# Optimization experiments

Hardware: AMD Instinct MI355X
Metric: run time of the kernel (lower is better)

Reference implementation:

```python
import jax, jax.numpy as jnp
import numpy as np

N_NODES = 50000
N_EDGES = 800000
D_IN = 128
D_HID = 128
D_OUT = 40
NUM_LAYERS = 2


def _sage_conv(x, src, dst, W_l, b_l, W_r, num_nodes):
    # PyG SAGEConv (aggr='mean'): out = lin_l(mean_{j in N(i)} x_j) + lin_r(x_i)
    msg = x[src]                                              # [E, d] gather
    agg = jax.ops.segment_sum(msg, dst, num_segments=num_nodes)  # [N, d] scatter-add
    deg = jax.ops.segment_sum(jnp.ones_like(dst, dtype=x.dtype), dst,
                              num_segments=num_nodes)
    agg = agg / jnp.clip(deg, 1.0)[:, None]                   # mean (deg>=1 clamp)
    return agg @ W_l.T + b_l + x @ W_r.T


def setup_inputs() -> dict:
    key = jax.random.key(0)
    ks = jax.random.split(key, 10)
    x = jax.random.normal(ks[0], (N_NODES, D_IN), dtype=jnp.float32)
    edge_index = jax.random.randint(ks[1], (2, N_EDGES), 0, N_NODES, dtype=jnp.int64)
    s = 1.0 / np.sqrt(D_IN)
    W1_l = jax.random.uniform(ks[2], (D_HID, D_IN), jnp.float32, -s, s)
    b1_l = jax.random.uniform(ks[3], (D_HID,), jnp.float32, -s, s)
    W1_r = jax.random.uniform(ks[4], (D_HID, D_IN), jnp.float32, -s, s)
    sh = 1.0 / np.sqrt(D_HID)
    W2_l = jax.random.uniform(ks[5], (D_HID, D_HID), jnp.float32, -sh, sh)
    b2_l = jax.random.uniform(ks[6], (D_HID,), jnp.float32, -sh, sh)
    W2_r = jax.random.uniform(ks[7], (D_HID, D_HID), jnp.float32, -sh, sh)
    sc = 1.0 / np.sqrt(D_HID * NUM_LAYERS)
    W_lin = jax.random.uniform(ks[8], (D_OUT, D_HID * NUM_LAYERS), jnp.float32, -sc, sc)
    b_lin = jax.random.uniform(ks[9], (D_OUT,), jnp.float32, -sc, sc)
    return {"x": x, "edge_index": edge_index,
            "W1_l": W1_l, "b1_l": b1_l, "W1_r": W1_r,
            "W2_l": W2_l, "b2_l": b2_l, "W2_r": W2_r,
            "W_lin": W_lin, "b_lin": b_lin}


def reference(x, edge_index, W1_l, b1_l, W1_r, W2_l, b2_l, W2_r, W_lin, b_lin):
    src, dst = edge_index[0], edge_index[1]
    n = x.shape[0]
    h1 = jax.nn.relu(_sage_conv(x, src, dst, W1_l, b1_l, W1_r, n))   # dropout: eval mode -> identity
    h2 = jax.nn.relu(_sage_conv(h1, src, dst, W2_l, b2_l, W2_r, n))
    h_cat = jnp.concatenate([h1, h2], axis=1)                        # [N, 2*hid]
    logits = h_cat @ W_lin.T + b_lin                                 # [N, out]
    return jax.nn.log_softmax(logits, axis=1)
```

## Files before the change

### kernel.cpp

```cpp
#include <hip/hip_runtime.h>
#include <math.h>

#define N_NODES 50000
#define N_EDGES 800000
#define D 128
#define NBLK 196
#define GATHER_BLOCKS 2048

typedef __attribute__((ext_vector_type(8))) short bf16x8;
typedef __attribute__((ext_vector_type(4))) float f32x4;
typedef __attribute__((ext_vector_type(4))) unsigned int u32x4;

static __device__ __forceinline__ unsigned short f2bf(float f) {
    unsigned int u = __float_as_uint(f);
    u = (u + 0x7fffu + ((u >> 16) & 1u)) >> 16;
    return (unsigned short)u;
}
static __device__ __forceinline__ float bf2f(unsigned short h) {
    return __uint_as_float(((unsigned int)h) << 16);
}

__global__ void prep_deg_kernel(const int* __restrict__ dst, int* __restrict__ deg,
                                int* __restrict__ rank,
                                const float* __restrict__ x,
                                const float* __restrict__ W1l, const float* __restrict__ W1r,
                                const float* __restrict__ W2l, const float* __restrict__ W2r,
                                const float* __restrict__ Wlin,
                                unsigned short* __restrict__ xhi, unsigned short* __restrict__ xlo,
                                unsigned short* __restrict__ W1hi, unsigned short* __restrict__ W1lo,
                                unsigned short* __restrict__ W2hi, unsigned short* __restrict__ W2lo,
                                unsigned short* __restrict__ WLhi, unsigned short* __restrict__ WLlo) {
    int b = blockIdx.x, tid = threadIdx.x;
    if (b < 3125) {
        int e = b * 256 + tid;
        rank[e] = atomicAdd(&deg[dst[e]], 1);
    } else if (b < 9375) {
        int i = ((b - 3125) * 256 + tid) * 4;
        float4 v = *(const float4*)(x + i);
        ushort4 h, l;
        h.x = f2bf(v.x); l.x = f2bf(v.x - bf2f(h.x));
        h.y = f2bf(v.y); l.y = f2bf(v.y - bf2f(h.y));
        h.z = f2bf(v.z); l.z = f2bf(v.z - bf2f(h.z));
        h.w = f2bf(v.w); l.w = f2bf(v.w - bf2f(h.w));
        *(ushort4*)(xhi + i) = h;
        *(ushort4*)(xlo + i) = l;
    } else if (b < 9503) {
        int isW2 = (b >= 9439);
        const float* A = isW2 ? W2l : W1l;
        const float* B = isW2 ? W2r : W1r;
        unsigned short* hi = isW2 ? W2hi : W1hi;
        unsigned short* lo = isW2 ? W2lo : W1lo;
        int f = (b - (isW2 ? 9439 : 9375)) * 2 + (tid >> 7);
        int t = tid & 127;
        float va = A[f * 128 + t], vb = B[f * 128 + t];
        unsigned short ha = f2bf(va), hb = f2bf(vb);
        hi[f * 256 + t]       = ha;
        hi[f * 256 + 128 + t] = hb;
        lo[f * 256 + t]       = f2bf(va - bf2f(ha));
        lo[f * 256 + 128 + t] = f2bf(vb - bf2f(hb));
    } else {
        int f = b - 9503;
        float v = (f < 40) ? Wlin[f * 256 + tid] : 0.f;
        unsigned short h = f2bf(v);
        WLhi[f * 256 + tid] = h;
        WLlo[f * 256 + tid] = f2bf(v - bf2f(h));
    }
}

__global__ void scan_partial(const int* __restrict__ deg, int* __restrict__ bsum) {
    __shared__ int wt[4];
    int tid = threadIdx.x, lane = tid & 63, wv = tid >> 6;
    int idx = blockIdx.x * 256 + tid;
    int v = (idx < N_NODES) ? deg[idx] : 0;
    int s = v;
    #pragma unroll
    for (int o = 1; o < 64; o <<= 1) s += __shfl_xor(s, o, 64);
    if (lane == 0) wt[wv] = s;
    __syncthreads();
    if (tid == 0) bsum[blockIdx.x] = wt[0] + wt[1] + wt[2] + wt[3];
}

__global__ void scan_write(const int* __restrict__ deg, const int* __restrict__ bsum,
                           int* __restrict__ rowptr) {
    __shared__ int wt[4], wt2[4];
    int tid = threadIdx.x, lane = tid & 63, wv = tid >> 6;
    int v0 = (tid < blockIdx.x) ? bsum[tid] : 0;
    int s0 = v0;
    #pragma unroll
    for (int o = 1; o < 64; o <<= 1) s0 += __shfl_xor(s0, o, 64);
    if (lane == 0) wt2[wv] = s0;
    int idx = blockIdx.x * 256 + tid;
    int v = (idx < N_NODES) ? deg[idx] : 0;
    int s = v;
    #pragma unroll
    for (int o = 1; o < 64; o <<= 1) { int t = __shfl_up(s, o, 64); if (lane >= o) s += t; }
    if (lane == 63) wt[wv] = s;
    __syncthreads();
    int boff = wt2[0] + wt2[1] + wt2[2] + wt2[3];
    #pragma unroll
    for (int w = 0; w < 4; w++) boff += (w < wv) ? wt[w] : 0;
    int excl = boff + s - v;
    if (idx < N_NODES) rowptr[idx] = excl;
    if (idx == 0) rowptr[N_NODES] = N_EDGES;
}

__global__ void bucket_kernel(const int* __restrict__ src, const int* __restrict__ dst,
                              const int* __restrict__ rowptr, const int* __restrict__ rank,
                              int* __restrict__ srcs_sorted) {
    int e = blockIdx.x * blockDim.x + threadIdx.x;
    if (e < N_EDGES) {
        srcs_sorted[rowptr[dst[e]] + rank[e]] = src[e];
    }
}

__global__ __launch_bounds__(256, 8) void gather_mean(
    const int* __restrict__ srcs, const int* __restrict__ rowptr,
    const unsigned short* __restrict__ Shi,
    unsigned short* __restrict__ Aghi, unsigned short* __restrict__ Aglo)
{
    const int tid = threadIdx.x;
    const int wv = tid >> 6, lane = tid & 63;
    const int g = lane >> 4, q = lane & 15;
    const int qb = q << 4;
    const char* xb = (const char*)Shi;
    const int wid = blockIdx.x * 4 + wv;
    const int NW = GATHER_BLOCKS * 4;
    #pragma unroll 1
    for (int p = wid; p < N_NODES / 2; p += NW) {
        const int nA = 2 * p, nB = 2 * p + 1;
        const int begA = rowptr[nA];
        const int endA = rowptr[nA + 1];
        const int endB = rowptr[nB + 1];
        const int begB = endA;
        const int degA = endA - begA, degB = endB - begB;
        float ax[4] = {0,0,0,0}, ay[4] = {0,0,0,0};
        float bx[4] = {0,0,0,0}, by[4] = {0,0,0,0};
        int nsA = (degA + 63) >> 6, nsB = (degB + 63) >> 6;
        int nsmax = max(nsA, nsB);
        #pragma unroll 1
        for (int st = 0; st < nsmax; st++) {
            int svA = 0, svB = 0, nbA = 0, nbB = 0;
            if (st < nsA) {
                int sb = begA + (st << 6);
                nbA = min(64, endA - sb);
                svA = srcs[min(sb + lane, endA - 1)];
            }
            if (st < nsB) {
                int sb = begB + (st << 6);
                nbB = min(64, endB - sb);
                svB = srcs[min(sb + lane, endB - 1)];
            }
            int itA = (nbA + 3) >> 2, itB = (nbB + 3) >> 2;
            int itmax = max(itA, itB);
            #pragma unroll 2
            for (int b = 0; b < itmax; b++) {
                int ei = (b << 2) + g;
                if (b < itA) {
                    unsigned sv = (unsigned)__shfl(svA, ei, 64);
                    u32x4 v = *(const u32x4*)(xb + ((sv << 8) + qb));
                    v.x = (ei < nbA) ? v.x : 0u;
                    v.y = (ei < nbA) ? v.y : 0u;
                    v.z = (ei < nbA) ? v.z : 0u;
                    v.w = (ei < nbA) ? v.w : 0u;
                    ax[0] += __uint_as_float(v.x << 16); ay[0] += __uint_as_float(v.x & 0xffff0000u);
                    ax[1] += __uint_as_float(v.y << 16); ay[1] += __uint_as_float(v.y & 0xffff0000u);
                    ax[2] += __uint_as_float(v.z << 16); ay[2] += __uint_as_float(v.z & 0xffff0000u);
                    ax[3] += __uint_as_float(v.w << 16); ay[3] += __uint_as_float(v.w & 0xffff0000u);
                }
                if (b < itB) {
                    unsigned sv = (unsigned)__shfl(svB, ei, 64);
                    u32x4 v = *(const u32x4*)(xb + ((sv << 8) + qb));
                    v.x = (ei < nbB) ? v.x : 0u;
                    v.y = (ei < nbB) ? v.y : 0u;
                    v.z = (ei < nbB) ? v.z : 0u;
                    v.w = (ei < nbB) ? v.w : 0u;
                    bx[0] += __uint_as_float(v.x << 16); by[0] += __uint_as_float(v.x & 0xffff0000u);
                    bx[1] += __uint_as_float(v.y << 16); by[1] += __uint_as_float(v.y & 0xffff0000u);
                    bx[2] += __uint_as_float(v.z << 16); by[2] += __uint_as_float(v.z & 0xffff0000u);
                    bx[3] += __uint_as_float(v.w << 16); by[3] += __uint_as_float(v.w & 0xffff0000u);
                }
            }
        }
        #pragma unroll
        for (int d = 0; d < 4; d++) {
            ax[d] += __shfl_xor(ax[d], 16, 64); ax[d] += __shfl_xor(ax[d], 32, 64);
            ay[d] += __shfl_xor(ay[d], 16, 64); ay[d] += __shfl_xor(ay[d], 32, 64);
            bx[d] += __shfl_xor(bx[d], 16, 64); bx[d] += __shfl_xor(bx[d], 32, 64);
            by[d] += __shfl_xor(by[d], 16, 64); by[d] += __shfl_xor(by[d], 32, 64);
        }
        if (g == 0) {
            float invA = 1.0f / fmaxf((float)degA, 1.0f);
            float invB = 1.0f / fmaxf((float)degB, 1.0f);
            u32x4 ha, la, hb, lb;
            #pragma unroll
            for (int d = 0; d < 4; d++) {
                float sx = ax[d] * invA, sy = ay[d] * invA;
                unsigned short h0 = f2bf(sx), h1 = f2bf(sy);
                unsigned short l0 = f2bf(sx - bf2f(h0)), l1 = f2bf(sy - bf2f(h1));
                ha[d] = (unsigned)h0 | ((unsigned)h1 << 16);
                la[d] = (unsigned)l0 | ((unsigned)l1 << 16);
                float tx = bx[d] * invB, ty = by[d] * invB;
                unsigned short h2 = f2bf(tx), h3 = f2bf(ty);
                unsigned short l2 = f2bf(tx - bf2f(h2)), l3 = f2bf(ty - bf2f(h3));
                hb[d] = (unsigned)h2 | ((unsigned)h3 << 16);
                lb[d] = (unsigned)l2 | ((unsigned)l3 << 16);
            }
            *(u32x4*)(Aghi + (size_t)nA * D + q * 8) = ha;
            *(u32x4*)(Aglo + (size_t)nA * D + q * 8) = la;
            *(u32x4*)(Aghi + (size_t)nB * D + q * 8) = hb;
            *(u32x4*)(Aglo + (size_t)nB * D + q * 8) = lb;
        }
    }
}

template<bool FINAL>
__global__ __launch_bounds__(256, 4) void gemm_layer(
    const unsigned short* __restrict__ Aghi, const unsigned short* __restrict__ Aglo,
    const unsigned short* __restrict__ A2hi, const unsigned short* __restrict__ A2lo,
    const unsigned short* __restrict__ Whi, const unsigned short* __restrict__ Wlo,
    const float* __restrict__ bias,
    unsigned short* __restrict__ Ohi, unsigned short* __restrict__ Olo,
    const unsigned short* __restrict__ WLhi, const unsigned short* __restrict__ WLlo,
    const float* __restrict__ blin, float* __restrict__ out)
{
    __shared__ unsigned short Wl[2][8192];

    const int tid = threadIdx.x;
    const int wv = tid >> 6, lane = tid & 63;
    const int nb0 = blockIdx.x * 32;
    const int m = lane & 15, quad = lane >> 4;
    const int gg = wv & 1, tp = wv >> 1;
    const int nodec = min(nb0 + gg * 16 + m, N_NODES - 1);

    bf16x8 a1h[4], a1l[4], a2h[4], a2l[4];
    {
        const unsigned short* r1h = Aghi + (size_t)nodec * D + quad * 8;
        const unsigned short* r1l = Aglo + (size_t)nodec * D + quad * 8;
        const unsigned short* r2h = A2hi + (size_t)nodec * D + quad * 8;
        const unsigned short* r2l = A2lo + (size_t)nodec * D + quad * 8;
        #pragma unroll
        for (int ks = 0; ks < 4; ks++) {
            a1h[ks] = *(const bf16x8*)(r1h + ks * 32);
            a1l[ks] = *(const bf16x8*)(r1l + ks * 32);
            a2h[ks] = *(const bf16x8*)(r2h + ks * 32);
            a2l[ks] = *(const bf16x8*)(r2l + ks * 32);
        }
    }
    #pragma unroll
    for (int ks = 0; ks < 4; ks++) {
        asm volatile("" : "+v"(a1h[ks]), "+v"(a1l[ks]), "+v"(a2h[ks]), "+v"(a2l[ks]));
    }

    #pragma unroll 1
    for (int fq = 0; fq < 4; fq++) {
        const int f0 = fq * 32;
        if (fq) __syncthreads();
        #pragma unroll
        for (int itS = 0; itS < 8; itS++) {
            int c = tid + itS * 256;
            int plane = c >> 10;
            int w3 = c & 1023;
            int nt = w3 >> 9, w2 = w3 & 511;
            int ks = w2 >> 6, lidx = w2 & 63;
            int mm = lidx >> 2, qq = lidx & 3;
            const unsigned short* base = plane ? Wlo : Whi;
            const unsigned short* gp = base + (size_t)(f0 + nt * 16 + mm) * 256 + ks * 32 + qq * 8;
            *(bf16x8*)&Wl[plane][(size_t)w3 * 8] = *(const bf16x8*)gp;
        }
        __syncthreads();

        int f = f0 + tp * 16 + m;
        f32x4 acc0 = {0.f, 0.f, 0.f, 0.f};
        f32x4 acc1 = {0.f, 0.f, 0.f, 0.f};
        f32x4 acc2 = {0.f, 0.f, 0.f, 0.f};
        #pragma unroll
        for (int ks = 0; ks < 8; ks++) {
            int idx = (((tp * 8 + ks) << 6) + (m * 4 + quad)) * 8;
            bf16x8 bh = *(const bf16x8*)&Wl[0][idx];
            bf16x8 bl = *(const bf16x8*)&Wl[1][idx];
            bf16x8 ah = (ks < 4) ? a1h[ks] : a2h[ks - 4];
            bf16x8 al = (ks < 4) ? a1l[ks] : a2l[ks - 4];
            acc0 = __builtin_amdgcn_mfma_f32_16x16x32_bf16(ah, bh, acc0, 0, 0, 0);
            acc1 = __builtin_amdgcn_mfma_f32_16x16x32_bf16(ah, bl, acc1, 0, 0, 0);
            acc2 = __builtin_amdgcn_mfma_f32_16x16x32_bf16(al, bh, acc2, 0, 0, 0);
        }
        float bv = bias[f];
        #pragma unroll
        for (int r = 0; r < 4; r++) {
            int lrow = gg * 16 + quad * 4 + r;
            int nrow = nb0 + lrow;
            float v = fmaxf((acc0[r] + (acc1[r] + acc2[r])) + bv, 0.f);
            unsigned short h = f2bf(v);
            unsigned short l = f2bf(v - bf2f(h));
            if (nrow < N_NODES) {
                Ohi[(size_t)nrow * D + f] = h;
                Olo[(size_t)nrow * D + f] = l;
            }
        }
    }

    if (!FINAL) return;

    __syncthreads();
    float* stats = (float*)Wl;
    bf16x8 a3h[4], a3l[4];
    {
        const unsigned short* r3h = Ohi + (size_t)nodec * D + quad * 8;
        const unsigned short* r3l = Olo + (size_t)nodec * D + quad * 8;
        #pragma unroll
        for (int ks = 0; ks < 4; ks++) {
            a3h[ks] = *(const bf16x8*)(r3h + ks * 32);
            a3l[ks] = *(const bf16x8*)(r3l + ks * 32);
        }
    }
    const int ntiles = (tp == 0) ? 2 : 1;
    float res[2][4];
    #pragma unroll
    for (int t = 0; t < 2; t++) {
        if (t >= ntiles) break;
        int nt = (tp == 0) ? t : 2;
        int f = nt * 16 + m;
        const unsigned short* whirow = WLhi + (size_t)f * 256 + quad * 8;
        const unsigned short* wlorow = WLlo + (size_t)f * 256 + quad * 8;
        f32x4 acc0 = {0.f, 0.f, 0.f, 0.f};
        f32x4 acc1 = {0.f, 0.f, 0.f, 0.f};
        f32x4 acc2 = {0.f, 0.f, 0.f, 0.f};
        #pragma unroll
        for (int ks = 0; ks < 8; ks++) {
            bf16x8 bh = *(const bf16x8*)(whirow + ks * 32);
            bf16x8 bl = *(const bf16x8*)(wlorow + ks * 32);
            bf16x8 ah = (ks < 4) ? a2h[ks] : a3h[ks - 4];
            bf16x8 al = (ks < 4) ? a2l[ks] : a3l[ks - 4];
            acc0 = __builtin_amdgcn_mfma_f32_16x16x32_bf16(ah, bh, acc0, 0, 0, 0);
            acc1 = __builtin_amdgcn_mfma_f32_16x16x32_bf16(ah, bl, acc1, 0, 0, 0);
            acc2 = __builtin_amdgcn_mfma_f32_16x16x32_bf16(al, bh, acc2, 0, 0, 0);
        }
        float bv = (f < 40) ? blin[f] : 0.f;
        #pragma unroll
        for (int r = 0; r < 4; r++) res[t][r] = (acc0[r] + (acc1[r] + acc2[r])) + bv;
    }
    #pragma unroll
    for (int r = 0; r < 4; r++) {
        float pm = -INFINITY;
        #pragma unroll
        for (int t = 0; t < 2; t++) {
            if (t >= ntiles) break;
            int f = ((tp == 0) ? t : 2) * 16 + m;
            if (f < 40) pm = fmaxf(pm, res[t][r]);
        }
        #pragma unroll
        for (int o = 8; o > 0; o >>= 1) pm = fmaxf(pm, __shfl_xor(pm, o, 64));
        if (m == 0) stats[tp * 64 + gg * 16 + quad * 4 + r] = pm;
    }
    __syncthreads();
    float gm[4];
    #pragma unroll
    for (int r = 0; r < 4; r++) {
        int row = gg * 16 + quad * 4 + r;
        gm[r] = fmaxf(stats[row], stats[64 + row]);
        float ps = 0.f;
        #pragma unroll
        for (int t = 0; t < 2; t++) {
            if (t >= ntiles) break;
            int f = ((tp == 0) ? t : 2) * 16 + m;
            if (f < 40) ps += expf(res[t][r] - gm[r]);
        }
        #pragma unroll
        for (int o = 8; o > 0; o >>= 1) ps += __shfl_xor(ps, o, 64);
        if (m == 0) stats[128 + tp * 64 + row] = ps;
    }
    __syncthreads();
    #pragma unroll
    for (int r = 0; r < 4; r++) {
        int row = gg * 16 + quad * 4 + r;
        int nrow = nb0 + row;
        if (nrow >= N_NODES) continue;
        float lse = gm[r] + logf(stats[128 + row] + stats[192 + row]);
        #pragma unroll
        for (int t = 0; t < 2; t++) {
            if (t >= ntiles) break;
            int f = ((tp == 0) ? t : 2) * 16 + m;
            if (f < 40) out[(size_t)nrow * 40 + f] = res[t][r] - lse;
        }
    }
}

extern "C" void kernel_launch(void* const* d_in, const int* in_sizes, int n_in,
                              void* d_out, int out_size, void* d_ws, size_t ws_size,
                              hipStream_t stream) {
    const float* x     = (const float*)d_in[0];
    const int*   ei    = (const int*)d_in[1];
    const int*   src   = ei;
    const int*   dst   = ei + N_EDGES;
    const float* W1_l  = (const float*)d_in[2];
    const float* b1_l  = (const float*)d_in[3];
    const float* W1_r  = (const float*)d_in[4];
    const float* W2_l  = (const float*)d_in[5];
    const float* b2_l  = (const float*)d_in[6];
    const float* W2_r  = (const float*)d_in[7];
    const float* W_lin = (const float*)d_in[8];
    const float* b_lin = (const float*)d_in[9];
    float* out = (float*)d_out;

    const size_t nd = (size_t)N_NODES * D;
    unsigned short* xhi  = (unsigned short*)d_ws;
    unsigned short* xlo  = xhi + nd;
    unsigned short* h1hi = xlo + nd;
    unsigned short* h1lo = h1hi + nd;
    unsigned short* W1hi = h1lo + nd;
    unsigned short* W1lo = W1hi + 128 * 256;
    unsigned short* W2hi = W1lo + 128 * 256;
    unsigned short* W2lo = W2hi + 128 * 256;
    unsigned short* WLhi = W2lo + 128 * 256;
    unsigned short* WLlo = WLhi + 48 * 256;
    int* deg    = (int*)(WLlo + 48 * 256);
    int* rowptr = deg + N_NODES;
    int* rank   = rowptr + N_NODES + 1;
    int* srcs_sorted = rank + N_EDGES;
    int* bsum   = srcs_sorted + N_EDGES;
    unsigned short* aghi = (unsigned short*)(bsum + NBLK);
    unsigned short* aglo = aghi + nd;
    unsigned short* h2hi = aglo + nd;
    unsigned short* h2lo = h2hi + nd;

    hipMemsetAsync(deg, 0, N_NODES * sizeof(int), stream);
    prep_deg_kernel<<<9551, 256, 0, stream>>>(dst, deg, rank, x, W1_l, W1_r, W2_l, W2_r, W_lin,
                                              xhi, xlo, W1hi, W1lo, W2hi, W2lo, WLhi, WLlo);

    scan_partial<<<NBLK, 256, 0, stream>>>(deg, bsum);
    scan_write<<<NBLK, 256, 0, stream>>>(deg, bsum, rowptr);
    bucket_kernel<<<(N_EDGES + 255) / 256, 256, 0, stream>>>(src, dst, rowptr, rank, srcs_sorted);

    const int lblk = (N_NODES + 31) / 32;

    gather_mean<<<GATHER_BLOCKS, 256, 0, stream>>>(srcs_sorted, rowptr, xhi, aghi, aglo);
    gemm_layer<false><<<lblk, 256, 0, stream>>>(aghi, aglo, xhi, xlo,
                                                W1hi, W1lo, b1_l, h1hi, h1lo,
                                                nullptr, nullptr, nullptr, nullptr);
    gather_mean<<<GATHER_BLOCKS, 256, 0, stream>>>(srcs_sorted, rowptr, h1hi, aghi, aglo);
    gemm_layer<true><<<lblk, 256, 0, stream>>>(aghi, aglo, h1hi, h1lo,
                                               W2hi, W2lo, b2_l, h2hi, h2lo,
                                               WLhi, WLlo, b_lin, out);
}
```

Measured before the change: 302.7 us.

## Make GEMM persistent per feature-quarter and split classifier into separate kernel

```diff
diff --git a/kernel.cpp b/kernel.cpp
--- a/kernel.cpp
+++ b/kernel.cpp
@@ -6,6 +6,8 @@
 #define D 128
 #define NBLK 196
 #define GATHER_BLOCKS 2048
+#define NTILES 1563
+#define GEMM_CHUNKS 256
 
 typedef __attribute__((ext_vector_type(8))) short bf16x8;
 typedef __attribute__((ext_vector_type(4))) float f32x4;
@@ -213,63 +215,60 @@
     }
 }
 
-template<bool FINAL>
 __global__ __launch_bounds__(256, 4) void gemm_layer(
     const unsigned short* __restrict__ Aghi, const unsigned short* __restrict__ Aglo,
     const unsigned short* __restrict__ A2hi, const unsigned short* __restrict__ A2lo,
     const unsigned short* __restrict__ Whi, const unsigned short* __restrict__ Wlo,
     const float* __restrict__ bias,
-    unsigned short* __restrict__ Ohi, unsigned short* __restrict__ Olo,
-    const unsigned short* __restrict__ WLhi, const unsigned short* __restrict__ WLlo,
-    const float* __restrict__ blin, float* __restrict__ out)
+    unsigned short* __restrict__ Ohi, unsigned short* __restrict__ Olo)
 {
     __shared__ unsigned short Wl[2][8192];
 
     const int tid = threadIdx.x;
     const int wv = tid >> 6, lane = tid & 63;
-    const int nb0 = blockIdx.x * 32;
     const int m = lane & 15, quad = lane >> 4;
     const int gg = wv & 1, tp = wv >> 1;
-    const int nodec = min(nb0 + gg * 16 + m, N_NODES - 1);
-
-    bf16x8 a1h[4], a1l[4], a2h[4], a2l[4];
-    {
-        const unsigned short* r1h = Aghi + (size_t)nodec * D + quad * 8;
-        const unsigned short* r1l = Aglo + (size_t)nodec * D + quad * 8;
-        const unsigned short* r2h = A2hi + (size_t)nodec * D + quad * 8;
-        const unsigned short* r2l = A2lo + (size_t)nodec * D + quad * 8;
-        #pragma unroll
-        for (int ks = 0; ks < 4; ks++) {
-            a1h[ks] = *(const bf16x8*)(r1h + ks * 32);
-            a1l[ks] = *(const bf16x8*)(r1l + ks * 32);
-            a2h[ks] = *(const bf16x8*)(r2h + ks * 32);
-            a2l[ks] = *(const bf16x8*)(r2l + ks * 32);
-        }
-    }
-    #pragma unroll
-    for (int ks = 0; ks < 4; ks++) {
-        asm volatile("" : "+v"(a1h[ks]), "+v"(a1l[ks]), "+v"(a2h[ks]), "+v"(a2l[ks]));
-    }
+    const int fq = blockIdx.x & 3;
+    const int chunk = blockIdx.x >> 2;
+    const int f0 = fq * 32;
+
+    #pragma unroll
+    for (int itS = 0; itS < 8; itS++) {
+        int c = tid + itS * 256;
+        int plane = c >> 10;
+        int w3 = c & 1023;
+        int nt = w3 >> 9, w2 = w3 & 511;
+        int ks = w2 >> 6, lidx = w2 & 63;
+        int mm = lidx >> 2, qq = lidx & 3;
+        const unsigned short* base = plane ? Wlo : Whi;
+        const unsigned short* gp = base + (size_t)(f0 + nt * 16 + mm) * 256 + ks * 32 + qq * 8;
+        *(bf16x8*)&Wl[plane][(size_t)w3 * 8] = *(const bf16x8*)gp;
+    }
+    __syncthreads();
+
+    const int f = f0 + tp * 16 + m;
+    const float bv = bias[f];
 
     #pragma unroll 1
-    for (int fq = 0; fq < 4; fq++) {
-        const int f0 = fq * 32;
-        if (fq) __syncthreads();
-        #pragma unroll
-        for (int itS = 0; itS < 8; itS++) {
-            int c = tid + itS * 256;
-            int plane = c >> 10;
-            int w3 = c & 1023;
-            int nt = w3 >> 9, w2 = w3 & 511;
-            int ks = w2 >> 6, lidx = w2 & 63;
-            int mm = lidx >> 2, qq = lidx & 3;
-            const unsigned short* base = plane ? Wlo : Whi;
-            const unsigned short* gp = base + (size_t)(f0 + nt * 16 + mm) * 256 + ks * 32 + qq * 8;
-            *(bf16x8*)&Wl[plane][(size_t)w3 * 8] = *(const bf16x8*)gp;
-        }
-        __syncthreads();
-
-        int f = f0 + tp * 16 + m;
+    for (int tile = chunk; tile < NTILES; tile += GEMM_CHUNKS) {
+        const int nb0 = tile * 32;
+        const int nodec = min(nb0 + gg * 16 + m, N_NODES - 1);
+
+        bf16x8 a1h[4], a1l[4], a2h[4], a2l[4];
+        {
+            const unsigned short* r1h = Aghi + (size_t)nodec * D + quad * 8;
+            const unsigned short* r1l = Aglo + (size_t)nodec * D + quad * 8;
+            const unsigned short* r2h = A2hi + (size_t)nodec * D + quad * 8;
+            const unsigned short* r2l = A2lo + (size_t)nodec * D + quad * 8;
+            #pragma unroll
+            for (int ks = 0; ks < 4; ks++) {
+                a1h[ks] = *(const bf16x8*)(r1h + ks * 32);
+                a1l[ks] = *(const bf16x8*)(r1l + ks * 32);
+                a2h[ks] = *(const bf16x8*)(r2h + ks * 32);
+                a2l[ks] = *(const bf16x8*)(r2l + ks * 32);
+            }
+        }
+
         f32x4 acc0 = {0.f, 0.f, 0.f, 0.f};
         f32x4 acc1 = {0.f, 0.f, 0.f, 0.f};
         f32x4 acc2 = {0.f, 0.f, 0.f, 0.f};
@@ -284,11 +283,9 @@
             acc1 = __builtin_amdgcn_mfma_f32_16x16x32_bf16(ah, bl, acc1, 0, 0, 0);
             acc2 = __builtin_amdgcn_mfma_f32_16x16x32_bf16(al, bh, acc2, 0, 0, 0);
         }
-        float bv = bias[f];
         #pragma unroll
         for (int r = 0; r < 4; r++) {
-            int lrow = gg * 16 + quad * 4 + r;
-            int nrow = nb0 + lrow;
+            int nrow = nb0 + gg * 16 + quad * 4 + r;
             float v = fmaxf((acc0[r] + (acc1[r] + acc2[r])) + bv, 0.f);
             unsigned short h = f2bf(v);
             unsigned short l = f2bf(v - bf2f(h));
@@ -298,17 +295,32 @@
             }
         }
     }
-
-    if (!FINAL) return;
-
-    __syncthreads();
-    float* stats = (float*)Wl;
-    bf16x8 a3h[4], a3l[4];
+}
+
+__global__ __launch_bounds__(256, 4) void classifier_kernel(
+    const unsigned short* __restrict__ H1hi, const unsigned short* __restrict__ H1lo,
+    const unsigned short* __restrict__ H2hi, const unsigned short* __restrict__ H2lo,
+    const unsigned short* __restrict__ WLhi, const unsigned short* __restrict__ WLlo,
+    const float* __restrict__ blin, float* __restrict__ out)
+{
+    __shared__ float stats[256];
+    const int tid = threadIdx.x;
+    const int wv = tid >> 6, lane = tid & 63;
+    const int nb0 = blockIdx.x * 32;
+    const int m = lane & 15, quad = lane >> 4;
+    const int gg = wv & 1, tp = wv >> 1;
+    const int nodec = min(nb0 + gg * 16 + m, N_NODES - 1);
+
+    bf16x8 a2h[4], a2l[4], a3h[4], a3l[4];
     {
-        const unsigned short* r3h = Ohi + (size_t)nodec * D + quad * 8;
-        const unsigned short* r3l = Olo + (size_t)nodec * D + quad * 8;
+        const unsigned short* r2h = H1hi + (size_t)nodec * D + quad * 8;
+        const unsigned short* r2l = H1lo + (size_t)nodec * D + quad * 8;
+        const unsigned short* r3h = H2hi + (size_t)nodec * D + quad * 8;
+        const unsigned short* r3l = H2lo + (size_t)nodec * D + quad * 8;
         #pragma unroll
         for (int ks = 0; ks < 4; ks++) {
+            a2h[ks] = *(const bf16x8*)(r2h + ks * 32);
+            a2l[ks] = *(const bf16x8*)(r2l + ks * 32);
             a3h[ks] = *(const bf16x8*)(r3h + ks * 32);
             a3l[ks] = *(const bf16x8*)(r3l + ks * 32);
         }
@@ -431,14 +443,12 @@
     scan_write<<<NBLK, 256, 0, stream>>>(deg, bsum, rowptr);
     bucket_kernel<<<(N_EDGES + 255) / 256, 256, 0, stream>>>(src, dst, rowptr, rank, srcs_sorted);
 
-    const int lblk = (N_NODES + 31) / 32;
-
     gather_mean<<<GATHER_BLOCKS, 256, 0, stream>>>(srcs_sorted, rowptr, xhi, aghi, aglo);
-    gemm_layer<false><<<lblk, 256, 0, stream>>>(aghi, aglo, xhi, xlo,
-                                                W1hi, W1lo, b1_l, h1hi, h1lo,
-                                                nullptr, nullptr, nullptr, nullptr);
+    gemm_layer<<<4 * GEMM_CHUNKS, 256, 0, stream>>>(aghi, aglo, xhi, xlo,
+                                                    W1hi, W1lo, b1_l, h1hi, h1lo);
     gather_mean<<<GATHER_BLOCKS, 256, 0, stream>>>(srcs_sorted, rowptr, h1hi, aghi, aglo);
-    gemm_layer<true><<<lblk, 256, 0, stream>>>(aghi, aglo, h1hi, h1lo,
-                                               W2hi, W2lo, b2_l, h2hi, h2lo,
-                                               WLhi, WLlo, b_lin, out);
-}
+    gemm_layer<<<4 * GEMM_CHUNKS, 256, 0, stream>>>(aghi, aglo, h1hi, h1lo,
+                                                    W2hi, W2lo, b2_l, h2hi, h2lo);
+    classifier_kernel<<<NTILES, 256, 0, stream>>>(h1hi, h1lo, h2hi, h2lo,
+                                                  WLhi, WLlo, b_lin, out);
+}
```

Result: slower. 349.2 us (+15.3%).

## Use persistent double-buffered GEMM for layer 1 with per-block weight slice

Applied to the files above, without the earlier changes.

```diff
diff --git a/kernel.cpp b/kernel.cpp
--- a/kernel.cpp
+++ b/kernel.cpp
@@ -6,6 +6,8 @@
 #define D 128
 #define NBLK 196
 #define GATHER_BLOCKS 2048
+#define NTILES 1563
+#define GEMM_CHUNKS 192
 
 typedef __attribute__((ext_vector_type(8))) short bf16x8;
 typedef __attribute__((ext_vector_type(4))) float f32x4;
@@ -213,8 +215,110 @@
     }
 }
 
-template<bool FINAL>
-__global__ __launch_bounds__(256, 4) void gemm_layer(
+#define LOADF(Fh1, Fl1, Fh2, Fl2, TILE) do {                                     \
+    int nb0_ = (TILE) * 32;                                                      \
+    int nodec_ = min(nb0_ + gg * 16 + m, N_NODES - 1);                           \
+    const unsigned short* r1h_ = Aghi + (size_t)nodec_ * D + quad * 8;           \
+    const unsigned short* r1l_ = Aglo + (size_t)nodec_ * D + quad * 8;           \
+    const unsigned short* r2h_ = A2hi + (size_t)nodec_ * D + quad * 8;           \
+    const unsigned short* r2l_ = A2lo + (size_t)nodec_ * D + quad * 8;           \
+    _Pragma("unroll")                                                            \
+    for (int ks_ = 0; ks_ < 4; ks_++) {                                          \
+        Fh1[ks_] = *(const bf16x8*)(r1h_ + ks_ * 32);                            \
+        Fl1[ks_] = *(const bf16x8*)(r1l_ + ks_ * 32);                            \
+        Fh2[ks_] = *(const bf16x8*)(r2h_ + ks_ * 32);                            \
+        Fl2[ks_] = *(const bf16x8*)(r2l_ + ks_ * 32);                            \
+    }                                                                            \
+} while (0)
+
+#define COMPST(Fh1, Fl1, Fh2, Fl2, TILE) do {                                    \
+    int nb0_ = (TILE) * 32;                                                      \
+    f32x4 acc0 = {0.f,0.f,0.f,0.f}, acc1 = {0.f,0.f,0.f,0.f}, acc2 = {0.f,0.f,0.f,0.f}; \
+    _Pragma("unroll")                                                            \
+    for (int ks_ = 0; ks_ < 8; ks_++) {                                          \
+        int idx_ = (((tp * 8 + ks_) << 6) + (m * 4 + quad)) * 8;                 \
+        bf16x8 bh_ = *(const bf16x8*)&Wl[0][idx_];                               \
+        bf16x8 bl_ = *(const bf16x8*)&Wl[1][idx_];                               \
+        bf16x8 ah_ = (ks_ < 4) ? Fh1[ks_] : Fh2[ks_ - 4];                        \
+        bf16x8 al_ = (ks_ < 4) ? Fl1[ks_] : Fl2[ks_ - 4];                        \
+        acc0 = __builtin_amdgcn_mfma_f32_16x16x32_bf16(ah_, bh_, acc0, 0, 0, 0); \
+        acc1 = __builtin_amdgcn_mfma_f32_16x16x32_bf16(ah_, bl_, acc1, 0, 0, 0); \
+        acc2 = __builtin_amdgcn_mfma_f32_16x16x32_bf16(al_, bh_, acc2, 0, 0, 0); \
+    }                                                                            \
+    _Pragma("unroll")                                                            \
+    for (int r_ = 0; r_ < 4; r_++) {                                             \
+        int nrow_ = nb0_ + gg * 16 + quad * 4 + r_;                              \
+        float v_ = fmaxf((acc0[r_] + (acc1[r_] + acc2[r_])) + bv, 0.f);          \
+        unsigned short h_ = f2bf(v_);                                            \
+        unsigned short l_ = f2bf(v_ - bf2f(h_));                                 \
+        if (nrow_ < N_NODES) {                                                   \
+            Ohi[(size_t)nrow_ * D + f] = h_;                                     \
+            Olo[(size_t)nrow_ * D + f] = l_;                                     \
+        }                                                                        \
+    }                                                                            \
+} while (0)
+
+__global__ __launch_bounds__(256, 3) void gemm_persist(
+    const unsigned short* __restrict__ Aghi, const unsigned short* __restrict__ Aglo,
+    const unsigned short* __restrict__ A2hi, const unsigned short* __restrict__ A2lo,
+    const unsigned short* __restrict__ Whi, const unsigned short* __restrict__ Wlo,
+    const float* __restrict__ bias,
+    unsigned short* __restrict__ Ohi, unsigned short* __restrict__ Olo)
+{
+    __shared__ unsigned short Wl[2][8192];
+
+    const int tid = threadIdx.x;
+    const int wv = tid >> 6, lane = tid & 63;
+    const int m = lane & 15, quad = lane >> 4;
+    const int gg = wv & 1, tp = wv >> 1;
+    const int fq = blockIdx.x & 3;
+    const int chunk = blockIdx.x >> 2;
+    const int f0 = fq * 32;
+
+    #pragma unroll
+    for (int itS = 0; itS < 8; itS++) {
+        int c = tid + itS * 256;
+        int plane = c >> 10;
+        int w3 = c & 1023;
+        int nt = w3 >> 9, w2 = w3 & 511;
+        int ks = w2 >> 6, lidx = w2 & 63;
+        int mm = lidx >> 2, qq = lidx & 3;
+        const unsigned short* base = plane ? Wlo : Whi;
+        const unsigned short* gp = base + (size_t)(f0 + nt * 16 + mm) * 256 + ks * 32 + qq * 8;
+        *(bf16x8*)&Wl[plane][(size_t)w3 * 8] = *(const bf16x8*)gp;
+    }
+    __syncthreads();
+
+    const int f = f0 + tp * 16 + m;
+    const float bv = bias[f];
+
+    bf16x8 Ph1[4], Pl1[4], Ph2[4], Pl2[4];
+    bf16x8 Qh1[4], Ql1[4], Qh2[4], Ql2[4];
+    int t = chunk;
+    LOADF(Ph1, Pl1, Ph2, Pl2, t);
+    #pragma unroll 1
+    while (true) {
+        int tn = t + GEMM_CHUNKS;
+        if (tn < NTILES) {
+            LOADF(Qh1, Ql1, Qh2, Ql2, tn);
+            COMPST(Ph1, Pl1, Ph2, Pl2, t);
+        } else {
+            COMPST(Ph1, Pl1, Ph2, Pl2, t);
+            break;
+        }
+        int tm = tn + GEMM_CHUNKS;
+        if (tm < NTILES) {
+            LOADF(Ph1, Pl1, Ph2, Pl2, tm);
+            COMPST(Qh1, Ql1, Qh2, Ql2, tn);
+        } else {
+            COMPST(Qh1, Ql1, Qh2, Ql2, tn);
+            break;
+        }
+        t = tm;
+    }
+}
+
+__global__ __launch_bounds__(256, 4) void gemm_fused(
     const unsigned short* __restrict__ Aghi, const unsigned short* __restrict__ Aglo,
     const unsigned short* __restrict__ A2hi, const unsigned short* __restrict__ A2lo,
     const unsigned short* __restrict__ Whi, const unsigned short* __restrict__ Wlo,
@@ -245,10 +349,6 @@
             a2h[ks] = *(const bf16x8*)(r2h + ks * 32);
             a2l[ks] = *(const bf16x8*)(r2l + ks * 32);
         }
-    }
-    #pragma unroll
-    for (int ks = 0; ks < 4; ks++) {
-        asm volatile("" : "+v"(a1h[ks]), "+v"(a1l[ks]), "+v"(a2h[ks]), "+v"(a2l[ks]));
     }
 
     #pragma unroll 1
@@ -298,8 +398,6 @@
             }
         }
     }
-
-    if (!FINAL) return;
 
     __syncthreads();
     float* stats = (float*)Wl;
@@ -431,14 +529,11 @@
     scan_write<<<NBLK, 256, 0, stream>>>(deg, bsum, rowptr);
     bucket_kernel<<<(N_EDGES + 255) / 256, 256, 0, stream>>>(src, dst, rowptr, rank, srcs_sorted);
 
-    const int lblk = (N_NODES + 31) / 32;
-
     gather_mean<<<GATHER_BLOCKS, 256, 0, stream>>>(srcs_sorted, rowptr, xhi, aghi, aglo);
-    gemm_layer<false><<<lblk, 256, 0, stream>>>(aghi, aglo, xhi, xlo,
-                                                W1hi, W1lo, b1_l, h1hi, h1lo,
-                                                nullptr, nullptr, nullptr, nullptr);
+    gemm_persist<<<4 * GEMM_CHUNKS, 256, 0, stream>>>(aghi, aglo, xhi, xlo,
+                                                      W1hi, W1lo, b1_l, h1hi, h1lo);
     gather_mean<<<GATHER_BLOCKS, 256, 0, stream>>>(srcs_sorted, rowptr, h1hi, aghi, aglo);
-    gemm_layer<true><<<lblk, 256, 0, stream>>>(aghi, aglo, h1hi, h1lo,
-                                               W2hi, W2lo, b2_l, h2hi, h2lo,
-                                               WLhi, WLlo, b_lin, out);
-}
+    gemm_fused<<<NTILES, 256, 0, stream>>>(aghi, aglo, h1hi, h1lo,
+                                           W2hi, W2lo, b2_l, h2hi, h2lo,
+                                           WLhi, WLlo, b_lin, out);
+}
```

Result: slower. 367.2 us (+21.3%).

## Use persistent weight-stationary GEMM for layer 1 split by feature quarter

Applied to the files above, without the earlier changes.

```diff
diff --git a/kernel.cpp b/kernel.cpp
--- a/kernel.cpp
+++ b/kernel.cpp
@@ -6,6 +6,8 @@
 #define D 128
 #define NBLK 196
 #define GATHER_BLOCKS 2048
+#define NTILES 1563
+#define GEMM_CHUNKS 256
 
 typedef __attribute__((ext_vector_type(8))) short bf16x8;
 typedef __attribute__((ext_vector_type(4))) float f32x4;
@@ -213,8 +215,89 @@
     }
 }
 
-template<bool FINAL>
-__global__ __launch_bounds__(256, 4) void gemm_layer(
+__global__ __launch_bounds__(256, 4) void gemm_persist(
+    const unsigned short* __restrict__ Aghi, const unsigned short* __restrict__ Aglo,
+    const unsigned short* __restrict__ A2hi, const unsigned short* __restrict__ A2lo,
+    const unsigned short* __restrict__ Whi, const unsigned short* __restrict__ Wlo,
+    const float* __restrict__ bias,
+    unsigned short* __restrict__ Ohi, unsigned short* __restrict__ Olo)
+{
+    __shared__ unsigned short Wl[2][8192];
+
+    const int tid = threadIdx.x;
+    const int wv = tid >> 6, lane = tid & 63;
+    const int m = lane & 15, quad = lane >> 4;
+    const int gg = wv & 1, tp = wv >> 1;
+    const int fq = blockIdx.x & 3;
+    const int chunk = blockIdx.x >> 2;
+    const int f0 = fq * 32;
+
+    #pragma unroll
+    for (int itS = 0; itS < 8; itS++) {
+        int c = tid + itS * 256;
+        int plane = c >> 10;
+        int w3 = c & 1023;
+        int nt = w3 >> 9, w2 = w3 & 511;
+        int ks = w2 >> 6, lidx = w2 & 63;
+        int mm = lidx >> 2, qq = lidx & 3;
+        const unsigned short* base = plane ? Wlo : Whi;
+        const unsigned short* gp = base + (size_t)(f0 + nt * 16 + mm) * 256 + ks * 32 + qq * 8;
+        *(bf16x8*)&Wl[plane][(size_t)w3 * 8] = *(const bf16x8*)gp;
+    }
+    __syncthreads();
+
+    const int f = f0 + tp * 16 + m;
+    const float bv = bias[f];
+
+    #pragma unroll 1
+    for (int tile = chunk; tile < NTILES; tile += GEMM_CHUNKS) {
+        const int nb0 = tile * 32;
+        const int nodec = min(nb0 + gg * 16 + m, N_NODES - 1);
+
+        bf16x8 a1h[4], a1l[4], a2h[4], a2l[4];
+        {
+            const unsigned short* r1h = Aghi + (size_t)nodec * D + quad * 8;
+            const unsigned short* r1l = Aglo + (size_t)nodec * D + quad * 8;
+            const unsigned short* r2h = A2hi + (size_t)nodec * D + quad * 8;
+            const unsigned short* r2l = A2lo + (size_t)nodec * D + quad * 8;
+            #pragma unroll
+            for (int ks = 0; ks < 4; ks++) {
+                a1h[ks] = *(const bf16x8*)(r1h + ks * 32);
+                a1l[ks] = *(const bf16x8*)(r1l + ks * 32);
+                a2h[ks] = *(const bf16x8*)(r2h + ks * 32);
+                a2l[ks] = *(const bf16x8*)(r2l + ks * 32);
+            }
+        }
+
+        f32x4 acc0 = {0.f, 0.f, 0.f, 0.f};
+        f32x4 acc1 = {0.f, 0.f, 0.f, 0.f};
+        f32x4 acc2 = {0.f, 0.f, 0.f, 0.f};
+        #pragma unroll
+        for (int ks = 0; ks < 8; ks++) {
+            int idx = (((tp * 8 + ks) << 6) + (m * 4 + quad)) * 8;
+            bf16x8 bh = *(const bf16x8*)&Wl[0][idx];
+            bf16x8 bl = *(const bf16x8*)&Wl[1][idx];
+            bf16x8 ah = (ks < 4) ? a1h[ks] : a2h[ks - 4];
+            bf16x8 al = (ks < 4) ? a1l[ks] : a2l[ks - 4];
+            acc0 = __builtin_amdgcn_mfma_f32_16x16x32_bf16(ah, bh, acc0, 0, 0, 0);
+            acc1 = __builtin_amdgcn_mfma_f32_16x16x32_bf16(ah, bl, acc1, 0, 0, 0);
+            acc2 = __builtin_amdgcn_mfma_f32_16x16x32_bf16(al, bh, acc2, 0, 0, 0);
+        }
+        #pragma unroll
+        for (int r = 0; r < 4; r++) {
+            int nrow = nb0 + gg * 16 + quad * 4 + r;
+            float v = fmaxf((acc0[r] + (acc1[r] + acc2[r])) + bv, 0.f);
+            unsigned short h = f2bf(v);
+            unsigned short l = f2bf(v - bf2f(h));
+            if (nrow < N_NODES) {
+                Ohi[(size_t)nrow * D + f] = h;
+                Olo[(size_t)nrow * D + f] = l;
+            }
+        }
+    }
+}
+
+__global__ __launch_bounds__(256, 4) void gemm_fused(
     const unsigned short* __restrict__ Aghi, const unsigned short* __restrict__ Aglo,
     const unsigned short* __restrict__ A2hi, const unsigned short* __restrict__ A2lo,
     const unsigned short* __restrict__ Whi, const unsigned short* __restrict__ Wlo,
@@ -245,10 +328,6 @@
             a2h[ks] = *(const bf16x8*)(r2h + ks * 32);
             a2l[ks] = *(const bf16x8*)(r2l + ks * 32);
         }
-    }
-    #pragma unroll
-    for (int ks = 0; ks < 4; ks++) {
-        asm volatile("" : "+v"(a1h[ks]), "+v"(a1l[ks]), "+v"(a2h[ks]), "+v"(a2l[ks]));
     }
 
     #pragma unroll 1
@@ -298,8 +377,6 @@
             }
         }
     }
-
-    if (!FINAL) return;
 
     __syncthreads();
     float* stats = (float*)Wl;
@@ -431,14 +508,11 @@
     scan_write<<<NBLK, 256, 0, stream>>>(deg, bsum, rowptr);
     bucket_kernel<<<(N_EDGES + 255) / 256, 256, 0, stream>>>(src, dst, rowptr, rank, srcs_sorted);
 
-    const int lblk = (N_NODES + 31) / 32;
-
     gather_mean<<<GATHER_BLOCKS, 256, 0, stream>>>(srcs_sorted, rowptr, xhi, aghi, aglo);
-    gemm_layer<false><<<lblk, 256, 0, stream>>>(aghi, aglo, xhi, xlo,
-                                                W1hi, W1lo, b1_l, h1hi, h1lo,
-                                                nullptr, nullptr, nullptr, nullptr);
+    gemm_persist<<<4 * GEMM_CHUNKS, 256, 0, stream>>>(aghi, aglo, xhi, xlo,
+                                                      W1hi, W1lo, b1_l, h1hi, h1lo);
     gather_mean<<<GATHER_BLOCKS, 256, 0, stream>>>(srcs_sorted, rowptr, h1hi, aghi, aglo);
-    gemm_layer<true><<<lblk, 256, 0, stream>>>(aghi, aglo, h1hi, h1lo,
-                                               W2hi, W2lo, b2_l, h2hi, h2lo,
-                                               WLhi, WLlo, b_lin, out);
-}
+    gemm_fused<<<NTILES, 256, 0, stream>>>(aghi, aglo, h1hi, h1lo,
+                                           W2hi, W2lo, b2_l, h2hi, h2lo,
+                                           WLhi, WLlo, b_lin, out);
+}
```

After: 322.2 us. 6.4% more time.
